# Kernel optimization log

Measured on AMD Instinct MI355X. Metric: run time of the kernel, lower is better.

## Reference

```python
import jax, jax.numpy as jnp
import numpy as np

HIDDEN = 256
HEADS = 8
HEAD_SIZE = HIDDEN // HEADS  # 32
CTX = 512
FF = 4 * HIDDEN
LN_EPS = 1e-5


def setup_inputs() -> dict:
    key = jax.random.key(0)
    ks = jax.random.split(key, 12)
    s = 0.02
    return {
        "x": jax.random.normal(ks[0], (32, CTX, HIDDEN), dtype=jnp.float32),
        # per-head Q/K/V projections, stored [H, D, E] ([in, out] orientation)
        "wq": jax.random.normal(ks[1], (HEADS, HIDDEN, HEAD_SIZE), dtype=jnp.float32) * s,
        "wk": jax.random.normal(ks[2], (HEADS, HIDDEN, HEAD_SIZE), dtype=jnp.float32) * s,
        "wv": jax.random.normal(ks[3], (HEADS, HIDDEN, HEAD_SIZE), dtype=jnp.float32) * s,
        "w_proj": jax.random.normal(ks[4], (HIDDEN, HIDDEN), dtype=jnp.float32) * s,
        "w1": jax.random.normal(ks[5], (HIDDEN, FF), dtype=jnp.float32) * s,
        "b1": jnp.zeros((FF,), dtype=jnp.float32),
        "w2": jax.random.normal(ks[6], (FF, HIDDEN), dtype=jnp.float32) * s,
        "b2": jnp.zeros((HIDDEN,), dtype=jnp.float32),
        "g_ln1": jnp.ones((HIDDEN,), dtype=jnp.float32),
        "be_ln1": jnp.zeros((HIDDEN,), dtype=jnp.float32),
        "g_ln2": jnp.ones((HIDDEN,), dtype=jnp.float32),
        "be_ln2": jnp.zeros((HIDDEN,), dtype=jnp.float32),
    }


def _layernorm(x, g, b):
    mu = jnp.mean(x, axis=-1, keepdims=True)
    var = jnp.var(x, axis=-1, keepdims=True)
    return (x - mu) * jax.lax.rsqrt(var + LN_EPS) * g + b


def reference(x, wq, wk, wv, w_proj, w1, b1, w2, b2, g_ln1, be_ln1, g_ln2, be_ln2):
    B, S, D = x.shape  # S == CTX
    # per-head projections: [B, H, S, E]
    q = jnp.einsum("bsd,hde->bhse", x, wq)
    k = jnp.einsum("bsd,hde->bhse", x, wk)
    v = jnp.einsum("bsd,hde->bhse", x, wv)
    scores = jnp.einsum("bhse,bhte->bhst", q, k) * (HEAD_SIZE ** -0.5)
    causal = jnp.tril(jnp.ones((S, S), dtype=bool))  # [S, S]
    scores = jnp.where(causal, scores, -jnp.inf)
    attn = jax.nn.softmax(scores, axis=-1)
    ctx = jnp.einsum("bhst,bhte->bhse", attn, v)
    ctx = ctx.transpose(0, 2, 1, 3).reshape(B, S, D)  # concat heads
    attn_out = ctx @ w_proj
    h = x + _layernorm(attn_out, g_ln1, be_ln1)
    ff = jax.nn.relu(h @ w1 + b1) @ w2 + b2
    return x + _layernorm(ff, g_ln2, be_ln2)
```

## Files before the change

kernel.cpp:

```cpp
#include <hip/hip_runtime.h>
#include <hip/hip_bf16.h>

#define B_   32
#define S_   512
#define D_   256
#define H_   8
#define E_   32
#define FF_  1024
#define T_   (B_ * S_)

typedef __attribute__((ext_vector_type(8))) short short8;
typedef __attribute__((ext_vector_type(4))) float f32x4;

static __device__ __forceinline__ unsigned short f2bf(float f) {
    union { float f; unsigned int u; } c; c.f = f;
    unsigned int u = c.u;
    u += 0x7fffu + ((u >> 16) & 1u);
    return (unsigned short)(u >> 16);
}
static __device__ __forceinline__ float bf2f(unsigned short u) {
    union { unsigned int u; float f; } c; c.u = ((unsigned int)u) << 16;
    return c.f;
}
static __device__ __forceinline__ unsigned int cvtpk(float lo, float hi) {
    unsigned int r;
    asm("v_cvt_pk_bf16_f32 %0, %1, %2" : "=v"(r) : "v"(lo), "v"(hi));
    return r;
}

#define GLOAD16(g, l) __builtin_amdgcn_global_load_lds( \
    (const __attribute__((address_space(1))) void*)(g), \
    (__attribute__((address_space(3))) void*)(l), 16, 0, 0)

__global__ void prep_kernel(const float* __restrict__ x,
                            const float* __restrict__ wq, const float* __restrict__ wk,
                            const float* __restrict__ wv, const float* __restrict__ w_proj,
                            const float* __restrict__ w1, const float* __restrict__ w2,
                            unsigned short* __restrict__ xb, unsigned short* __restrict__ Wqkv,
                            unsigned short* __restrict__ Wproj, unsigned short* __restrict__ W1t,
                            unsigned short* __restrict__ W2t) {
    int blk = blockIdx.x, tid = threadIdx.x;
    if (blk < 4096) {
        int i = blk * 256 + tid;
        float4 v = *(const float4*)&x[(size_t)i * 4];
        ushort4 o; o.x = f2bf(v.x); o.y = f2bf(v.y); o.z = f2bf(v.z); o.w = f2bf(v.w);
        *(ushort4*)&xb[(size_t)i * 4] = o;
    } else if (blk < 4864) {
        int idx = (blk - 4096) * 256 + tid;
        int nn = idx >> 8, k = idx & 255;
        int which = nn >> 8, r = nn & 255, h = r >> 5, e = r & 31;
        const float* w = (which == 0) ? wq : (which == 1 ? wk : wv);
        float v = w[(h * D_ + k) * E_ + e];
        if (which == 0) v *= 0.17677669529663687f * 1.4426950408889634f;
        Wqkv[idx] = f2bf(v);
    } else if (blk < 5120) {
        int idx = (blk - 4864) * 256 + tid;
        int nn = idx >> 8, k = idx & 255;
        Wproj[idx] = f2bf(w_proj[(size_t)k * 256 + nn]);
    } else if (blk < 6144) {
        int idx = (blk - 5120) * 256 + tid;
        int nn = idx >> 8, k = idx & 255;
        W1t[idx] = f2bf(w1[(size_t)k * 1024 + nn]);
    } else {
        int idx = (blk - 6144) * 256 + tid;
        int nn = idx >> 10, k = idx & 1023;
        W2t[idx] = f2bf(w2[(size_t)k * 256 + nn]);
    }
}

template <int EP, int BN>
__global__ __launch_bounds__(256) void gemm_mfma(const unsigned short* __restrict__ A,
                                                 const unsigned short* __restrict__ Bt,
                                                 const float* __restrict__ bias,
                                                 void* __restrict__ Cout,
                                                 unsigned short* __restrict__ Vout,
                                                 int M, int N, int K) {
    constexpr int FN = BN / 32;
    __shared__ char smem[16384 + BN * 128];
    const int tid = threadIdx.x;
    const int bm = blockIdx.y * 128, bn = blockIdx.x * BN;
    const int wave = tid >> 6, lane = tid & 63;
    const int l15 = lane & 15, kc = lane >> 4;
    const int wr = (wave >> 1) * 64, wc = (wave & 1) * (BN / 2);

    auto stage = [&](int buf, int kt) {
        int k0 = kt * 32;
        char* aBase = smem + buf * 8192;
        char* bBase = smem + 16384 + buf * (BN * 64);
        #pragma unroll
        for (int j = 0; j < 2; ++j) {
            int o = j * 256 + tid;
            int r = o >> 2, c = o & 3;
            int g = c ^ ((r >> 1) & 3);
            GLOAD16(A + (size_t)(bm + r) * K + k0 + g * 8, aBase + o * 16);
        }
        #pragma unroll
        for (int j = 0; j < BN / 64; ++j) {
            int o = j * 256 + tid;
            int r = o >> 2, c = o & 3;
            int g = c ^ ((r >> 1) & 3);
            GLOAD16(Bt + (size_t)(bn + r) * K + k0 + g * 8, bBase + o * 16);
        }
    };

    f32x4 acc[4][FN];
    #pragma unroll
    for (int m = 0; m < 4; ++m)
        #pragma unroll
        for (int n = 0; n < FN; ++n) acc[m][n] = (f32x4){0.f, 0.f, 0.f, 0.f};

    const int NT = K >> 5;
    stage(0, 0);
    __syncthreads();

    int buf = 0;
    for (int kt = 0; kt < NT; ++kt) {
        if (kt + 1 < NT) stage(buf ^ 1, kt + 1);
        const char* aBase = smem + buf * 8192;
        const char* bBase = smem + 16384 + buf * (BN * 64);
        short8 afr[4], bfr[FN];
        #pragma unroll
        for (int m = 0; m < 4; ++m) {
            int row = wr + m * 16 + l15;
            int cc = kc ^ ((row >> 1) & 3);
            afr[m] = *(const short8*)(aBase + row * 64 + cc * 16);
        }
        #pragma unroll
        for (int n = 0; n < FN; ++n) {
            int row = wc + n * 16 + l15;
            int cc = kc ^ ((row >> 1) & 3);
            bfr[n] = *(const short8*)(bBase + row * 64 + cc * 16);
        }
        #pragma unroll
        for (int m = 0; m < 4; ++m)
            #pragma unroll
            for (int n = 0; n < FN; ++n)
                acc[m][n] = __builtin_amdgcn_mfma_f32_16x16x32_bf16(afr[m], bfr[n], acc[m][n], 0, 0, 0);
        __syncthreads();
        buf ^= 1;
    }

    if (EP & 8) {
        #pragma unroll
        for (int n = 0; n < FN; ++n) {
            int col = bn + wc + n * 16 + l15;
            if (col < 512) {
                #pragma unroll
                for (int m = 0; m < 4; ++m) {
                    int row0 = bm + wr + m * 16 + kc * 4;
                    #pragma unroll
                    for (int j = 0; j < 4; ++j)
                        ((unsigned short*)Cout)[(size_t)(row0 + j) * 512 + col] = f2bf(acc[m][n][j]);
                }
            } else {
                int hh = (col - 512) >> 5, e = (col - 512) & 31;
                #pragma unroll
                for (int m = 0; m < 4; ++m) {
                    int row0 = bm + wr + m * 16 + kc * 4;
                    int bb = row0 >> 9, s0 = row0 & 511;
                    ushort4 o4;
                    o4.x = f2bf(acc[m][n][0]); o4.y = f2bf(acc[m][n][1]);
                    o4.z = f2bf(acc[m][n][2]); o4.w = f2bf(acc[m][n][3]);
                    *(ushort4*)&Vout[(size_t)(bb * 8 + hh) * 16384 + e * 512 + s0] = o4;
                }
            }
        }
    } else {
        #pragma unroll
        for (int n = 0; n < FN; ++n) {
            int col = bn + wc + n * 16 + l15;
            float bv = (EP & 1) ? bias[col] : 0.f;
            #pragma unroll
            for (int m = 0; m < 4; ++m) {
                int row0 = bm + wr + m * 16 + kc * 4;
                #pragma unroll
                for (int j = 0; j < 4; ++j) {
                    float v = acc[m][n][j] + bv;
                    if (EP & 2) v = fmaxf(v, 0.f);
                    if (EP & 4) ((unsigned short*)Cout)[(size_t)(row0 + j) * N + col] = f2bf(v);
                    else        ((float*)Cout)[(size_t)(row0 + j) * N + col] = v;
                }
            }
        }
    }
}

template <int BIAS, int OUTF32>
__global__ __launch_bounds__(256) void gemm_ln2(const unsigned short* __restrict__ A,
                                                const unsigned short* __restrict__ Bt,
                                                const float* __restrict__ bias,
                                                const float* __restrict__ xres,
                                                const float* __restrict__ gw,
                                                const float* __restrict__ bw,
                                                void* __restrict__ Cout,
                                                int K) {
    __shared__ char smem[40960];
    __shared__ float sred[2][2][64];
    const int tid = threadIdx.x;
    const int bm = blockIdx.x * 64;
    const int wave = tid >> 6, lane = tid & 63;
    const int l15 = lane & 15, kc = lane >> 4;
    const int wr = (wave >> 1) * 32, wc = (wave & 1) * 128;

    auto stage = [&](int buf, int kt) {
        int k0 = kt * 32;
        char* aBase = smem + buf * 4096;
        char* bBase = smem + 8192 + buf * 16384;
        {
            int o = tid;
            int r = o >> 2, c = o & 3;
            int g = c ^ ((r >> 1) & 3);
            GLOAD16(A + (size_t)(bm + r) * K + k0 + g * 8, aBase + o * 16);
        }
        #pragma unroll
        for (int j = 0; j < 4; ++j) {
            int o = j * 256 + tid;
            int r = o >> 2, c = o & 3;
            int g = c ^ ((r >> 1) & 3);
            GLOAD16(Bt + (size_t)r * K + k0 + g * 8, bBase + o * 16);
        }
    };

    f32x4 acc[2][8];
    #pragma unroll
    for (int m = 0; m < 2; ++m)
        #pragma unroll
        for (int n = 0; n < 8; ++n) acc[m][n] = (f32x4){0.f, 0.f, 0.f, 0.f};

    const int NT = K >> 5;
    stage(0, 0);
    __syncthreads();

    int buf = 0;
    for (int kt = 0; kt < NT; ++kt) {
        if (kt + 1 < NT) stage(buf ^ 1, kt + 1);
        const char* aBase = smem + buf * 4096;
        const char* bBase = smem + 8192 + buf * 16384;
        short8 afr[2], bfr[8];
        #pragma unroll
        for (int m = 0; m < 2; ++m) {
            int row = wr + m * 16 + l15;
            int cc = kc ^ ((row >> 1) & 3);
            afr[m] = *(const short8*)(aBase + row * 64 + cc * 16);
        }
        #pragma unroll
        for (int n = 0; n < 8; ++n) {
            int row = wc + n * 16 + l15;
            int cc = kc ^ ((row >> 1) & 3);
            bfr[n] = *(const short8*)(bBase + row * 64 + cc * 16);
        }
        #pragma unroll
        for (int m = 0; m < 2; ++m)
            #pragma unroll
            for (int n = 0; n < 8; ++n)
                acc[m][n] = __builtin_amdgcn_mfma_f32_16x16x32_bf16(afr[m], bfr[n], acc[m][n], 0, 0, 0);
        __syncthreads();
        buf ^= 1;
    }

    float gv[8], bev[8];
    #pragma unroll
    for (int n = 0; n < 8; ++n) {
        int col = wc + n * 16 + l15;
        gv[n] = gw[col]; bev[n] = bw[col];
        if (BIAS) {
            float bb = bias[col];
            #pragma unroll
            for (int m = 0; m < 2; ++m)
                #pragma unroll
                for (int j = 0; j < 4; ++j) acc[m][n][j] += bb;
        }
    }

    #pragma unroll
    for (int m = 0; m < 2; ++m) {
        #pragma unroll
        for (int j = 0; j < 4; ++j) {
            float s = 0.f, s2 = 0.f;
            #pragma unroll
            for (int n = 0; n < 8; ++n) { float v = acc[m][n][j]; s += v; s2 += v * v; }
            #pragma unroll
            for (int off = 1; off < 16; off <<= 1) {
                s += __shfl_xor(s, off); s2 += __shfl_xor(s2, off);
            }
            if (l15 == 0) {
                int rl = wr + m * 16 + kc * 4 + j;
                sred[wave & 1][0][rl] = s;
                sred[wave & 1][1][rl] = s2;
            }
        }
    }
    __syncthreads();

    #pragma unroll
    for (int m = 0; m < 2; ++m) {
        #pragma unroll
        for (int j = 0; j < 4; ++j) {
            int rl = wr + m * 16 + kc * 4 + j;
            float stot  = sred[0][0][rl] + sred[1][0][rl];
            float s2tot = sred[0][1][rl] + sred[1][1][rl];
            float mu  = stot * (1.f / 256.f);
            float var = s2tot * (1.f / 256.f) - mu * mu;
            float rr  = rsqrtf(var + 1e-5f);
            int rowg = bm + rl;
            #pragma unroll
            for (int n = 0; n < 8; ++n) {
                int col = wc + n * 16 + l15;
                float o = xres[(size_t)rowg * 256 + col] + (acc[m][n][j] - mu) * rr * gv[n] + bev[n];
                if (OUTF32) ((float*)Cout)[(size_t)rowg * 256 + col] = o;
                else ((unsigned short*)Cout)[(size_t)rowg * 256 + col] = f2bf(o);
            }
        }
    }
}

__global__ __launch_bounds__(256, 2) void attn_mfma(const unsigned short* __restrict__ qk,
                                                    const unsigned short* __restrict__ vtg,
                                                    unsigned short* __restrict__ ctx) {
    __shared__ unsigned short klds[512 * 32];
    __shared__ unsigned short vlds[32 * 512];
    __shared__ unsigned short plds[4][32 * 64];
    const int blk = blockIdx.x;
    const int bh = blk >> 1, qh = blk & 1;
    const int b = bh >> 3, h = bh & 7;
    const int tid = threadIdx.x;
    const int wave = tid >> 6, lane = tid & 63;
    const int l15 = lane & 15, kc = lane >> 4;

    const unsigned short* kg = qk + (size_t)b * 512 * 512 + 256 + h * 32;
    #pragma unroll
    for (int it = 0; it < 8; ++it) {
        int slot = it * 256 + tid;
        int r = slot >> 2, c = slot & 3;
        GLOAD16(kg + (size_t)r * 512 + (c ^ ((r >> 1) & 3)) * 8, (char*)klds + slot * 16);
    }
    #pragma unroll
    for (int it = 0; it < 8; ++it) {
        int slot = it * 256 + tid;
        int e = slot >> 6, c = slot & 63;
        GLOAD16(vtg + (size_t)bh * 16384 + e * 512 + (c ^ (e & 7)) * 8,
                (char*)vlds + slot * 16);
    }

    const int cA = qh * 4 + wave, cB = 15 - cA;
    const int ntA = (cA >> 1) + 1, ntB = (cB >> 1) + 1;
    short8 qfA[2], qfB[2];
    #pragma unroll
    for (int qm = 0; qm < 2; ++qm) {
        qfA[qm] = *(const short8*)(qk + (size_t)(b * 512 + cA * 32 + qm * 16 + l15) * 512 + h * 32 + kc * 8);
        qfB[qm] = *(const short8*)(qk + (size_t)(b * 512 + cB * 32 + qm * 16 + l15) * 512 + h * 32 + kc * 8);
    }
    __syncthreads();

    unsigned short* pw = plds[wave];
    const int xsw = (l15 & 7) << 1;

    f32x4 OA[2][2], OB[2][2];
    float lA[2] = {0.f, 0.f}, lB[2] = {0.f, 0.f};
    #pragma unroll
    for (int qm = 0; qm < 2; ++qm) {
        OA[qm][0] = (f32x4){0.f, 0.f, 0.f, 0.f}; OA[qm][1] = (f32x4){0.f, 0.f, 0.f, 0.f};
        OB[qm][0] = (f32x4){0.f, 0.f, 0.f, 0.f}; OB[qm][1] = (f32x4){0.f, 0.f, 0.f, 0.f};
    }

    auto chunk_step = [&](const short8* qf, f32x4 (&O)[2][2], float* lreg,
                          int cc_, bool diag, const short8* kf, int t0) {
        #pragma unroll
        for (int qm = 0; qm < 2; ++qm) {
            f32x4 st[4];
            __builtin_amdgcn_s_setprio(1);
            #pragma unroll
            for (int tn = 0; tn < 4; ++tn)
                st[tn] = __builtin_amdgcn_mfma_f32_16x16x32_bf16(kf[tn], qf[qm],
                                                                 (f32x4){0.f, 0.f, 0.f, 0.f}, 0, 0, 0);
            __builtin_amdgcn_s_setprio(0);
            if (diag) {
                int qg = cc_ * 32 + qm * 16 + l15;
                #pragma unroll
                for (int tn = 0; tn < 4; ++tn)
                    #pragma unroll
                    for (int j = 0; j < 4; ++j)
                        if (t0 + tn * 16 + kc * 4 + j > qg) st[tn][j] = -1e30f;
            }
            float psum = 0.f;
            #pragma unroll
            for (int tn = 0; tn < 4; ++tn) {
                float p0 = __builtin_amdgcn_exp2f(st[tn][0]);
                float p1 = __builtin_amdgcn_exp2f(st[tn][1]);
                float p2 = __builtin_amdgcn_exp2f(st[tn][2]);
                float p3 = __builtin_amdgcn_exp2f(st[tn][3]);
                psum += (p0 + p1) + (p2 + p3);
                uint2 w;
                w.x = cvtpk(p0, p1);
                w.y = cvtpk(p2, p3);
                int tc = (tn * 4 + kc) ^ xsw;
                *(uint2*)(pw + (qm * 16 + l15) * 64 + tc * 4) = w;
            }
            psum += __shfl_xor(psum, 16);
            psum += __shfl_xor(psum, 32);
            lreg[qm] += psum;
        }
        #pragma unroll
        for (int tt = 0; tt < 2; ++tt) {
            short8 pa[2];
            #pragma unroll
            for (int qm = 0; qm < 2; ++qm) {
                int tcr = (tt * 8 + kc * 2) ^ xsw;
                pa[qm] = *(const short8*)(pw + (qm * 16 + l15) * 64 + tcr * 4);
            }
            short8 vt[2];
            #pragma unroll
            for (int n = 0; n < 2; ++n) {
                int e = n * 16 + l15;
                int c = ((t0 >> 3) + tt * 4 + kc) ^ (e & 7);
                vt[n] = *(const short8*)(vlds + e * 512 + c * 8);
            }
            __builtin_amdgcn_s_setprio(1);
            #pragma unroll
            for (int qm = 0; qm < 2; ++qm)
                #pragma unroll
                for (int n = 0; n < 2; ++n)
                    O[qm][n] = __builtin_amdgcn_mfma_f32_16x16x32_bf16(pa[qm], vt[n], O[qm][n], 0, 0, 0);
            __builtin_amdgcn_s_setprio(0);
        }
    };

    for (int ti = 0; ti < ntB; ++ti) {
        const int t0 = ti * 64;
        short8 kf[4];
        #pragma unroll
        for (int tn = 0; tn < 4; ++tn) {
            int row = t0 + tn * 16 + l15;
            int cx = kc ^ ((row >> 1) & 3);
            kf[tn] = *(const short8*)((const char*)klds + row * 64 + cx * 16);
        }
        if (ti < ntA) chunk_step(qfA, OA, lA, cA, ti == ntA - 1, kf, t0);
        chunk_step(qfB, OB, lB, cB, ti == ntB - 1, kf, t0);
    }

    auto epilogue = [&](f32x4 (&O)[2][2], float* lreg, int cc_) {
        #pragma unroll
        for (int qm = 0; qm < 2; ++qm) {
            float linv = 1.f / lreg[qm];
            #pragma unroll
            for (int j = 0; j < 4; ++j) {
                float lj = __shfl(linv, kc * 4 + j, 16);
                size_t base = (size_t)(b * 512 + cc_ * 32 + qm * 16 + kc * 4 + j) * 256 + h * 32;
                ctx[base + l15]      = f2bf(O[qm][0][j] * lj);
                ctx[base + 16 + l15] = f2bf(O[qm][1][j] * lj);
            }
        }
    };
    epilogue(OA, lA, cA);
    epilogue(OB, lB, cB);
}

extern "C" void kernel_launch(void* const* d_in, const int* in_sizes, int n_in,
                              void* d_out, int out_size, void* d_ws, size_t ws_size,
                              hipStream_t stream) {
    (void)in_sizes; (void)n_in; (void)out_size; (void)ws_size;
    const float* x      = (const float*)d_in[0];
    const float* wq     = (const float*)d_in[1];
    const float* wk     = (const float*)d_in[2];
    const float* wv     = (const float*)d_in[3];
    const float* w_proj = (const float*)d_in[4];
    const float* w1     = (const float*)d_in[5];
    const float* b1     = (const float*)d_in[6];
    const float* w2     = (const float*)d_in[7];
    const float* b2     = (const float*)d_in[8];
    const float* g1     = (const float*)d_in[9];
    const float* be1    = (const float*)d_in[10];
    const float* g2     = (const float*)d_in[11];
    const float* be2    = (const float*)d_in[12];
    float* out = (float*)d_out;

    char* W = (char*)d_ws;
    unsigned short* qk      = (unsigned short*)(W + 0);
    unsigned short* vtg     = (unsigned short*)(W + 16777216);
    unsigned short* xb      = (unsigned short*)(W + 25165824);
    unsigned short* ctx     = (unsigned short*)(W + 25165824);
    unsigned short* hbuf    = (unsigned short*)(W + 33554432);
    unsigned short* ff1     = (unsigned short*)(W + 0);
    unsigned short* Wqkv_t  = (unsigned short*)(W + 50331648);
    unsigned short* Wproj_t = (unsigned short*)(W + 50724864);
    unsigned short* W1_t    = (unsigned short*)(W + 50855936);
    unsigned short* W2_t    = (unsigned short*)(W + 51380224);

    prep_kernel<<<7168, 256, 0, stream>>>(x, wq, wk, wv, w_proj, w1, w2,
                                          xb, Wqkv_t, Wproj_t, W1_t, W2_t);

    gemm_mfma<8, 128><<<dim3(6, T_ / 128), 256, 0, stream>>>(xb, Wqkv_t, nullptr, qk, vtg, T_, 768, 256);

    attn_mfma<<<B_ * H_ * 2, 256, 0, stream>>>(qk, vtg, ctx);

    gemm_ln2<0, 0><<<T_ / 64, 256, 0, stream>>>(ctx, Wproj_t, nullptr, x, g1, be1, hbuf, 256);

    gemm_mfma<7, 128><<<dim3(8, T_ / 128), 256, 0, stream>>>(hbuf, W1_t, b1, ff1, nullptr, T_, FF_, 256);

    gemm_ln2<1, 1><<<T_ / 64, 256, 0, stream>>>(ff1, W2_t, b2, x, g2, be2, out, 1024);
}
```

Measured before the change: 116.7 us.

## Prefetch two K-tiles ahead with fine-grained vmcnt waits in GEMM kernels

Restructures the double-buffered GEMM main loops so global-to-LDS loads for tile kt+2 are issued right after the current tile's fragments are read into registers. Full __syncthreads are replaced by explicit vmcnt/lgkmcnt waits plus raw barriers, which keeps one tile's loads in flight across the MFMA block. It also raises wave priority around the MFMA section. The hand-counted vmcnt values must match the number of GLOAD16s per stage, which is fragile and could race if the counts are wrong.

```diff
diff --git a/kernel.cpp b/kernel.cpp
--- a/kernel.cpp
+++ b/kernel.cpp
@@ -76,6 +76,7 @@
                                                  unsigned short* __restrict__ Vout,
                                                  int M, int N, int K) {
     constexpr int FN = BN / 32;
+    constexpr int NLD = 2 + BN / 64;
     __shared__ char smem[16384 + BN * 128];
     const int tid = threadIdx.x;
     const int bm = blockIdx.y * 128, bn = blockIdx.x * BN;
@@ -111,13 +112,15 @@
 
     const int NT = K >> 5;
     stage(0, 0);
-    __syncthreads();
-
-    int buf = 0;
+    stage(1, 1);
+    if (NLD == 3) asm volatile("s_waitcnt vmcnt(3)" ::: "memory");
+    else          asm volatile("s_waitcnt vmcnt(4)" ::: "memory");
+    __builtin_amdgcn_s_barrier();
+
     for (int kt = 0; kt < NT; ++kt) {
-        if (kt + 1 < NT) stage(buf ^ 1, kt + 1);
-        const char* aBase = smem + buf * 8192;
-        const char* bBase = smem + 16384 + buf * (BN * 64);
+        const int cur = kt & 1;
+        const char* aBase = smem + cur * 8192;
+        const char* bBase = smem + 16384 + cur * (BN * 64);
         short8 afr[4], bfr[FN];
         #pragma unroll
         for (int m = 0; m < 4; ++m) {
@@ -131,13 +134,27 @@
             int cc = kc ^ ((row >> 1) & 3);
             bfr[n] = *(const short8*)(bBase + row * 64 + cc * 16);
         }
+        asm volatile("s_waitcnt lgkmcnt(0)" ::: "memory");
+        __builtin_amdgcn_s_barrier();
+        if (kt + 2 < NT) stage(cur, kt + 2);
+
+        __builtin_amdgcn_s_setprio(1);
         #pragma unroll
         for (int m = 0; m < 4; ++m)
             #pragma unroll
             for (int n = 0; n < FN; ++n)
                 acc[m][n] = __builtin_amdgcn_mfma_f32_16x16x32_bf16(afr[m], bfr[n], acc[m][n], 0, 0, 0);
-        __syncthreads();
-        buf ^= 1;
+        __builtin_amdgcn_s_setprio(0);
+
+        if (kt + 1 < NT) {
+            if (kt + 2 < NT) {
+                if (NLD == 3) asm volatile("s_waitcnt vmcnt(3)" ::: "memory");
+                else          asm volatile("s_waitcnt vmcnt(4)" ::: "memory");
+            } else {
+                asm volatile("s_waitcnt vmcnt(0)" ::: "memory");
+            }
+            __builtin_amdgcn_s_barrier();
+        }
     }
 
     if (EP & 8) {
@@ -229,13 +246,14 @@
 
     const int NT = K >> 5;
     stage(0, 0);
-    __syncthreads();
-
-    int buf = 0;
+    stage(1, 1);
+    asm volatile("s_waitcnt vmcnt(5)" ::: "memory");
+    __builtin_amdgcn_s_barrier();
+
     for (int kt = 0; kt < NT; ++kt) {
-        if (kt + 1 < NT) stage(buf ^ 1, kt + 1);
-        const char* aBase = smem + buf * 4096;
-        const char* bBase = smem + 8192 + buf * 16384;
+        const int cur = kt & 1;
+        const char* aBase = smem + cur * 4096;
+        const char* bBase = smem + 8192 + cur * 16384;
         short8 afr[2], bfr[8];
         #pragma unroll
         for (int m = 0; m < 2; ++m) {
@@ -249,13 +267,23 @@
             int cc = kc ^ ((row >> 1) & 3);
             bfr[n] = *(const short8*)(bBase + row * 64 + cc * 16);
         }
+        asm volatile("s_waitcnt lgkmcnt(0)" ::: "memory");
+        __builtin_amdgcn_s_barrier();
+        if (kt + 2 < NT) stage(cur, kt + 2);
+
+        __builtin_amdgcn_s_setprio(1);
         #pragma unroll
         for (int m = 0; m < 2; ++m)
             #pragma unroll
             for (int n = 0; n < 8; ++n)
                 acc[m][n] = __builtin_amdgcn_mfma_f32_16x16x32_bf16(afr[m], bfr[n], acc[m][n], 0, 0, 0);
-        __syncthreads();
-        buf ^= 1;
+        __builtin_amdgcn_s_setprio(0);
+
+        if (kt + 1 < NT) {
+            if (kt + 2 < NT) asm volatile("s_waitcnt vmcnt(5)" ::: "memory");
+            else             asm volatile("s_waitcnt vmcnt(0)" ::: "memory");
+            __builtin_amdgcn_s_barrier();
+        }
     }
 
     float gv[8], bev[8];
```

Result: faster. 111.2 us (-4.7%).
